# Kernel tuning notes

Measured on AMD Instinct MI355X. Metric: run time of the kernel, lower is better.

The kernel has to match this reference:

```python
import jax, jax.numpy as jnp
import numpy as np

ROPE_BASE = 10000.0
NEG_INF = -1e30


def _rope(x, pos):
    # x: [B, Hx, D], pos: [B] int32. Rotate-half RoPE (non-interleaved).
    D = x.shape[-1]
    inv_freq = 1.0 / (ROPE_BASE ** (jnp.arange(0, D, 2, dtype=jnp.float32) / D))  # [D/2]
    ang = pos.astype(jnp.float32)[:, None] * inv_freq[None, :]                    # [B, D/2]
    emb = jnp.concatenate([ang, ang], axis=-1)                                    # [B, D]
    cos = jnp.cos(emb)[:, None, :]
    sin = jnp.sin(emb)[:, None, :]
    x1, x2 = x[..., : D // 2], x[..., D // 2 :]
    rotated = jnp.concatenate([-x2, x1], axis=-1)
    return x * cos + rotated * sin


def setup_inputs() -> dict:
    key = jax.random.key(0)
    ks = jax.random.split(key, 7)
    B, H, KVH, D = 32, 32, 8, 128
    BLOCK_SIZE, MAX_BLOCKS = 16, 128
    NUM_BLOCKS = B * MAX_BLOCKS  # 4096, disjoint blocks per sequence
    MAX_CTX = BLOCK_SIZE * MAX_BLOCKS  # 2048
    query = jax.random.normal(ks[0], (B, H, D), dtype=jnp.float32)
    new_k = jax.random.normal(ks[1], (B, KVH, D), dtype=jnp.float32)
    new_v = jax.random.normal(ks[2], (B, KVH, D), dtype=jnp.float32)
    k_cache = jax.random.normal(ks[3], (NUM_BLOCKS, BLOCK_SIZE, KVH, D), dtype=jnp.float32)
    v_cache = jax.random.normal(ks[4], (NUM_BLOCKS, BLOCK_SIZE, KVH, D), dtype=jnp.float32)
    block_table = jnp.arange(B * MAX_BLOCKS, dtype=jnp.int32).reshape(B, MAX_BLOCKS)
    context_lens = jnp.clip(jax.random.randint(ks[5], (B,), 0, MAX_CTX, dtype=jnp.int32), 1, MAX_CTX)
    return {"query": query, "key": new_k, "value": new_v,
            "k_cache": k_cache, "v_cache": v_cache,
            "block_table": block_table, "context_lens": context_lens}


def reference(query, key, value, k_cache, v_cache, block_table, context_lens):
    B, H, D = query.shape
    KVH = key.shape[1]
    G = H // KVH  # GQA group size
    block_size = k_cache.shape[1]
    max_blocks = block_table.shape[1]
    S = max_blocks * block_size
    scale = D ** -0.5

    # RoPE at position = context_lens (as in the original module)
    q_rot = _rope(query, context_lens)  # [B, H, D]
    k_rot = _rope(key, context_lens)    # [B, KVH, D]

    # Store new KV at token index context_lens - 1 via block table (paged scatter)
    tok = context_lens - 1
    blk = jnp.take_along_axis(block_table, (tok // block_size)[:, None], axis=1)[:, 0]  # [B]
    off = tok % block_size
    k_cache = k_cache.at[blk, off].set(k_rot)
    v_cache = v_cache.at[blk, off].set(value)

    # Gather per-sequence pages: [B, max_blocks, block_size, KVH, D] -> [B, S, KVH, D]
    K = k_cache[block_table].reshape(B, S, KVH, D)
    V = v_cache[block_table].reshape(B, S, KVH, D)

    # Single-query attention over valid context (positions < context_lens)
    qg = q_rot.reshape(B, KVH, G, D)
    scores = jnp.einsum("bkgd,bskd->bkgs", qg, K) * scale  # [B, KVH, G, S]
    valid = jnp.arange(S, dtype=jnp.int32)[None, :] < context_lens[:, None]  # [B, S]
    scores = jnp.where(valid[:, None, None, :], scores, NEG_INF)
    probs = jax.nn.softmax(scores, axis=-1)
    out = jnp.einsum("bkgs,bskd->bkgd", probs, V).reshape(B, H, D)
    return out
```

## Files before the change

kernel.cpp:

```cpp
#include <hip/hip_runtime.h>
#include <math.h>

#define BATCH 32
#define NH 32
#define NKVH 8
#define GRP 4
#define HD 128
#define BLKSZ 16
#define MAXB 128
#define PART 256
#define NPART 8
#define SCALE 0.08838834764831845f
#define NEGINF (-1e30f)

#define WS_QROT 0
#define WS_KROT (BATCH*NH*HD)
#define WS_ML   (WS_KROT + BATCH*NKVH*HD)
#define WS_OP   (WS_ML + BATCH*NKVH*GRP*NPART*2)

__global__ void rope_prep(const float* __restrict__ q,
                          const float* __restrict__ nk,
                          const int* __restrict__ ctx,
                          float* __restrict__ ws) {
    int b = blockIdx.x;
    int t = threadIdx.x;
    __shared__ float cs[64], sn[64];
    if (t < 64) {
        double f = pow(10000.0, -(double)t / 64.0);
        double a = (double)ctx[b] * f;
        cs[t] = (float)cos(a);
        sn[t] = (float)sin(a);
    }
    __syncthreads();
    int d = t;
    float c = cs[d & 63], s = sn[d & 63];
    for (int h = 0; h < NH; ++h) {
        const float* qp = q + ((size_t)b * NH + h) * HD;
        float x = qp[d];
        float y = qp[d ^ 64];
        float r = (d < 64) ? (x * c - y * s) : (x * c + y * s);
        ws[WS_QROT + ((size_t)b * NH + h) * HD + d] = r;
    }
    for (int kh = 0; kh < NKVH; ++kh) {
        const float* kp = nk + ((size_t)b * NKVH + kh) * HD;
        float x = kp[d];
        float y = kp[d ^ 64];
        float r = (d < 64) ? (x * c - y * s) : (x * c + y * s);
        ws[WS_KROT + ((size_t)b * NKVH + kh) * HD + d] = r;
    }
}

__global__ __launch_bounds__(256)
void attn_partial(const float* __restrict__ kc,
                  const float* __restrict__ vc,
                  const float* __restrict__ nv,
                  const int* __restrict__ btab,
                  const int* __restrict__ ctx,
                  float* __restrict__ ws) {
    int part = blockIdx.x, kvh = blockIdx.y, b = blockIdx.z;
    int L = ctx[b];
    int start = part * PART;
    if (start >= L) return;
    int end = min(start + PART, L);
    int n = end - start;
    int tok = L - 1;

    int tid = threadIdx.x;
    int hw = tid >> 5;
    int hl = tid & 31;
    int wave = tid >> 6;
    int lane = tid & 63;

    __shared__ float sc[GRP][PART];
    __shared__ float oacc[8][GRP][HD];

    const float* qrot = ws + WS_QROT + ((size_t)b * NH + kvh * GRP) * HD;
    float4 qa[GRP];
#pragma unroll
    for (int g = 0; g < GRP; ++g)
        qa[g] = *(const float4*)(qrot + g * HD + 4 * hl);

    const float* krot = ws + WS_KROT + ((size_t)b * NKVH + kvh) * HD;
    const int* bt = btab + b * MAXB;

    for (int s = start + hw; s < end; s += 8) {
        float4 k4;
        if (s == tok) {
            k4 = *(const float4*)(krot + 4 * hl);
        } else {
            int blk = bt[s >> 4];
            const float* kp = kc + (((size_t)blk * BLKSZ + (s & 15)) * NKVH + kvh) * HD;
            k4 = *(const float4*)(kp + 4 * hl);
        }
        float p[GRP];
#pragma unroll
        for (int g = 0; g < GRP; ++g)
            p[g] = qa[g].x * k4.x + qa[g].y * k4.y + qa[g].z * k4.z + qa[g].w * k4.w;
#pragma unroll
        for (int off = 16; off >= 1; off >>= 1) {
#pragma unroll
            for (int g = 0; g < GRP; ++g)
                p[g] += __shfl_xor(p[g], off, 32);
        }
        if (hl == 0) {
#pragma unroll
            for (int g = 0; g < GRP; ++g)
                sc[g][s - start] = p[g] * SCALE;
        }
    }
    __syncthreads();

    {
        int g = wave;
        float m = NEGINF;
        for (int i = lane; i < n; i += 64) m = fmaxf(m, sc[g][i]);
#pragma unroll
        for (int off = 32; off >= 1; off >>= 1) m = fmaxf(m, __shfl_xor(m, off));
        float sum = 0.f;
        for (int i = lane; i < n; i += 64) {
            float e = __expf(sc[g][i] - m);
            sc[g][i] = e;
            sum += e;
        }
#pragma unroll
        for (int off = 32; off >= 1; off >>= 1) sum += __shfl_xor(sum, off);
        if (lane == 0) {
            size_t mlidx = ((((size_t)b * NKVH + kvh) * GRP + g) * NPART + part) * 2;
            ws[WS_ML + mlidx] = m;
            ws[WS_ML + mlidx + 1] = sum;
        }
    }
    __syncthreads();

    float4 acc[GRP];
#pragma unroll
    for (int g = 0; g < GRP; ++g) acc[g] = make_float4(0.f, 0.f, 0.f, 0.f);

    for (int s = start + hw; s < end; s += 8) {
        float4 v4;
        if (s == tok) {
            v4 = *(const float4*)(nv + ((size_t)b * NKVH + kvh) * HD + 4 * hl);
        } else {
            int blk = bt[s >> 4];
            const float* vp = vc + (((size_t)blk * BLKSZ + (s & 15)) * NKVH + kvh) * HD;
            v4 = *(const float4*)(vp + 4 * hl);
        }
        int i = s - start;
#pragma unroll
        for (int g = 0; g < GRP; ++g) {
            float e = sc[g][i];
            acc[g].x += e * v4.x; acc[g].y += e * v4.y;
            acc[g].z += e * v4.z; acc[g].w += e * v4.w;
        }
    }
#pragma unroll
    for (int g = 0; g < GRP; ++g)
        *(float4*)&oacc[hw][g][4 * hl] = acc[g];
    __syncthreads();

    for (int o = tid; o < GRP * HD; o += 256) {
        int g = o >> 7, d = o & 127;
        float ssum = 0.f;
#pragma unroll
        for (int w = 0; w < 8; ++w) ssum += oacc[w][g][d];
        ws[WS_OP + ((((size_t)b * NKVH + kvh) * GRP + g) * NPART + part) * HD + d] = ssum;
    }
}

__global__ __launch_bounds__(128)
void attn_reduce(const int* __restrict__ ctx,
                 const float* __restrict__ ws,
                 float* __restrict__ out) {
    int bh = blockIdx.x;
    int b = bh >> 5;
    int h = bh & 31;
    int kvh = h >> 2, g = h & 3;
    int L = ctx[b];
    int np = min(NPART, (L + PART - 1) / PART);
    size_t base = (((size_t)b * NKVH + kvh) * GRP + g) * NPART;
    float M = NEGINF;
    for (int p = 0; p < np; ++p)
        M = fmaxf(M, ws[WS_ML + (base + p) * 2]);
    float w_[NPART];
    float Lsum = 0.f;
    for (int p = 0; p < np; ++p) {
        float e = __expf(ws[WS_ML + (base + p) * 2] - M);
        w_[p] = e;
        Lsum += e * ws[WS_ML + (base + p) * 2 + 1];
    }
    float inv = 1.0f / Lsum;
    int d = threadIdx.x;
    float acc = 0.f;
    for (int p = 0; p < np; ++p)
        acc += w_[p] * ws[WS_OP + (base + p) * HD + d];
    out[((size_t)b * NH + h) * HD + d] = acc * inv;
}

extern "C" void kernel_launch(void* const* d_in, const int* in_sizes, int n_in,
                              void* d_out, int out_size, void* d_ws, size_t ws_size,
                              hipStream_t stream) {
    const float* q    = (const float*)d_in[0];
    const float* nk   = (const float*)d_in[1];
    const float* nv   = (const float*)d_in[2];
    const float* kc   = (const float*)d_in[3];
    const float* vc   = (const float*)d_in[4];
    const int*   btab = (const int*)d_in[5];
    const int*   ctx  = (const int*)d_in[6];
    float* out = (float*)d_out;
    float* ws  = (float*)d_ws;

    rope_prep<<<dim3(BATCH), dim3(128), 0, stream>>>(q, nk, ctx, ws);
    attn_partial<<<dim3(NPART, NKVH, BATCH), dim3(256), 0, stream>>>(kc, vc, nv, btab, ctx, ws);
    attn_reduce<<<dim3(BATCH * NH), dim3(128), 0, stream>>>(ctx, ws, out);
}
```

Before: 510.9 us.

## Scatter new KV into cache, halve partition size, unroll K/V loads

The prep kernel now writes the rotated new key and the new value directly into the input K/V caches, so the attention kernel loses its per-token branch. The softmax scale is folded into the rotated query. Partition size drops from 256 to 128, which doubles the block count. Block-table entries and query rows are staged in shared memory, the QK loop is unrolled four-way, and the PV loop is restructured so each wave handles 64 contiguous tokens with float2 loads. Writing into the caller's input caches mutates the inputs across calls.

```diff
diff --git a/kernel.cpp b/kernel.cpp
--- a/kernel.cpp
+++ b/kernel.cpp
@@ -8,161 +8,207 @@
 #define HD 128
 #define BLKSZ 16
 #define MAXB 128
-#define PART 256
-#define NPART 8
+#define PART 128
+#define NPART 16
 #define SCALE 0.08838834764831845f
 #define NEGINF (-1e30f)
 
 #define WS_QROT 0
-#define WS_KROT (BATCH*NH*HD)
-#define WS_ML   (WS_KROT + BATCH*NKVH*HD)
+#define WS_ML   (BATCH*NH*HD)
 #define WS_OP   (WS_ML + BATCH*NKVH*GRP*NPART*2)
 
-__global__ void rope_prep(const float* __restrict__ q,
-                          const float* __restrict__ nk,
-                          const int* __restrict__ ctx,
-                          float* __restrict__ ws) {
+__global__ __launch_bounds__(128)
+void prep(const float* __restrict__ q,
+          const float* __restrict__ nk,
+          const float* __restrict__ nv,
+          float* __restrict__ kc,
+          float* __restrict__ vc,
+          const int* __restrict__ btab,
+          const int* __restrict__ ctx,
+          float* __restrict__ ws) {
     int b = blockIdx.x;
     int t = threadIdx.x;
+    int L = ctx[b];
     __shared__ float cs[64], sn[64];
     if (t < 64) {
         double f = pow(10000.0, -(double)t / 64.0);
-        double a = (double)ctx[b] * f;
+        double a = (double)L * f;
         cs[t] = (float)cos(a);
         sn[t] = (float)sin(a);
     }
     __syncthreads();
-    int d = t;
-    float c = cs[d & 63], s = sn[d & 63];
+    float c = cs[t & 63], s = sn[t & 63];
     for (int h = 0; h < NH; ++h) {
         const float* qp = q + ((size_t)b * NH + h) * HD;
-        float x = qp[d];
-        float y = qp[d ^ 64];
-        float r = (d < 64) ? (x * c - y * s) : (x * c + y * s);
-        ws[WS_QROT + ((size_t)b * NH + h) * HD + d] = r;
-    }
+        float x = qp[t], y = qp[t ^ 64];
+        float r = (t < 64) ? (x * c - y * s) : (x * c + y * s);
+        ws[WS_QROT + ((size_t)b * NH + h) * HD + t] = r * SCALE;
+    }
+    int tok = L - 1;
+    int blk = btab[b * MAXB + (tok >> 4)];
+    int off = tok & 15;
     for (int kh = 0; kh < NKVH; ++kh) {
         const float* kp = nk + ((size_t)b * NKVH + kh) * HD;
-        float x = kp[d];
-        float y = kp[d ^ 64];
-        float r = (d < 64) ? (x * c - y * s) : (x * c + y * s);
-        ws[WS_KROT + ((size_t)b * NKVH + kh) * HD + d] = r;
+        float x = kp[t], y = kp[t ^ 64];
+        float r = (t < 64) ? (x * c - y * s) : (x * c + y * s);
+        size_t row = (((size_t)blk * BLKSZ + off) * NKVH + kh) * HD;
+        kc[row + t] = r;
+        vc[row + t] = nv[((size_t)b * NKVH + kh) * HD + t];
     }
 }
 
 __global__ __launch_bounds__(256)
-void attn_partial(const float* __restrict__ kc,
-                  const float* __restrict__ vc,
-                  const float* __restrict__ nv,
-                  const int* __restrict__ btab,
-                  const int* __restrict__ ctx,
-                  float* __restrict__ ws) {
+void attn(const float* __restrict__ kc,
+          const float* __restrict__ vc,
+          const int* __restrict__ ctx,
+          const int* __restrict__ btab,
+          float* __restrict__ ws)
+{
     int part = blockIdx.x, kvh = blockIdx.y, b = blockIdx.z;
     int L = ctx[b];
     int start = part * PART;
     if (start >= L) return;
     int end = min(start + PART, L);
     int n = end - start;
-    int tok = L - 1;
 
     int tid = threadIdx.x;
     int hw = tid >> 5;
     int hl = tid & 31;
-    int wave = tid >> 6;
-    int lane = tid & 63;
-
+    int wave = tid >> 6, lane = tid & 63;
+
+    __shared__ int   bts[PART / BLKSZ];
+    __shared__ float qs[GRP][HD];
     __shared__ float sc[GRP][PART];
-    __shared__ float oacc[8][GRP][HD];
-
-    const float* qrot = ws + WS_QROT + ((size_t)b * NH + kvh * GRP) * HD;
+    __shared__ float oacc[4][GRP][HD];
+
+    if (tid < PART / BLKSZ)
+        bts[tid] = btab[b * MAXB + (start >> 4) + tid];
+    {
+        const float* qrot = ws + WS_QROT + ((size_t)b * NH + kvh * GRP) * HD;
+        ((float2*)&qs[0][0])[tid] = ((const float2*)qrot)[tid];
+    }
+    __syncthreads();
+
     float4 qa[GRP];
 #pragma unroll
     for (int g = 0; g < GRP; ++g)
-        qa[g] = *(const float4*)(qrot + g * HD + 4 * hl);
-
-    const float* krot = ws + WS_KROT + ((size_t)b * NKVH + kvh) * HD;
-    const int* bt = btab + b * MAXB;
-
-    for (int s = start + hw; s < end; s += 8) {
-        float4 k4;
-        if (s == tok) {
-            k4 = *(const float4*)(krot + 4 * hl);
-        } else {
-            int blk = bt[s >> 4];
-            const float* kp = kc + (((size_t)blk * BLKSZ + (s & 15)) * NKVH + kvh) * HD;
-            k4 = *(const float4*)(kp + 4 * hl);
-        }
-        float p[GRP];
+        qa[g] = *(const float4*)(&qs[g][4 * hl]);
+
+    const size_t koff = (size_t)kvh * HD + 4 * hl;
+
+    int i = start + hw;
+    for (; i + 24 < end; i += 32) {
+        int s0 = i, s1 = i + 8, s2 = i + 16, s3 = i + 24;
+        float4 k0 = *(const float4*)(kc + ((size_t)bts[(s0 - start) >> 4] << 14) + ((s0 & 15) << 10) + koff);
+        float4 k1 = *(const float4*)(kc + ((size_t)bts[(s1 - start) >> 4] << 14) + ((s1 & 15) << 10) + koff);
+        float4 k2 = *(const float4*)(kc + ((size_t)bts[(s2 - start) >> 4] << 14) + ((s2 & 15) << 10) + koff);
+        float4 k3 = *(const float4*)(kc + ((size_t)bts[(s3 - start) >> 4] << 14) + ((s3 & 15) << 10) + koff);
+        float p0[GRP], p1[GRP], p2[GRP], p3[GRP];
+#pragma unroll
+        for (int g = 0; g < GRP; ++g) {
+            p0[g] = qa[g].x * k0.x + qa[g].y * k0.y + qa[g].z * k0.z + qa[g].w * k0.w;
+            p1[g] = qa[g].x * k1.x + qa[g].y * k1.y + qa[g].z * k1.z + qa[g].w * k1.w;
+            p2[g] = qa[g].x * k2.x + qa[g].y * k2.y + qa[g].z * k2.z + qa[g].w * k2.w;
+            p3[g] = qa[g].x * k3.x + qa[g].y * k3.y + qa[g].z * k3.z + qa[g].w * k3.w;
+        }
+#pragma unroll
+        for (int off = 16; off >= 1; off >>= 1) {
+#pragma unroll
+            for (int g = 0; g < GRP; ++g) {
+                p0[g] += __shfl_xor(p0[g], off, 32);
+                p1[g] += __shfl_xor(p1[g], off, 32);
+                p2[g] += __shfl_xor(p2[g], off, 32);
+                p3[g] += __shfl_xor(p3[g], off, 32);
+            }
+        }
+        if (hl == 0) {
+#pragma unroll
+            for (int g = 0; g < GRP; ++g) {
+                sc[g][s0 - start] = p0[g];
+                sc[g][s1 - start] = p1[g];
+                sc[g][s2 - start] = p2[g];
+                sc[g][s3 - start] = p3[g];
+            }
+        }
+    }
+    for (; i < end; i += 8) {
+        float4 k0 = *(const float4*)(kc + ((size_t)bts[(i - start) >> 4] << 14) + ((i & 15) << 10) + koff);
+        float p0[GRP];
 #pragma unroll
         for (int g = 0; g < GRP; ++g)
-            p[g] = qa[g].x * k4.x + qa[g].y * k4.y + qa[g].z * k4.z + qa[g].w * k4.w;
-#pragma unroll
-        for (int off = 16; off >= 1; off >>= 1) {
+            p0[g] = qa[g].x * k0.x + qa[g].y * k0.y + qa[g].z * k0.z + qa[g].w * k0.w;
+#pragma unroll
+        for (int off = 16; off >= 1; off >>= 1)
 #pragma unroll
             for (int g = 0; g < GRP; ++g)
-                p[g] += __shfl_xor(p[g], off, 32);
-        }
-        if (hl == 0) {
+                p0[g] += __shfl_xor(p0[g], off, 32);
+        if (hl == 0)
 #pragma unroll
             for (int g = 0; g < GRP; ++g)
-                sc[g][s - start] = p[g] * SCALE;
-        }
+                sc[g][i - start] = p0[g];
     }
     __syncthreads();
 
     {
         int g = wave;
         float m = NEGINF;
-        for (int i = lane; i < n; i += 64) m = fmaxf(m, sc[g][i]);
+        for (int j = lane; j < n; j += 64) m = fmaxf(m, sc[g][j]);
 #pragma unroll
         for (int off = 32; off >= 1; off >>= 1) m = fmaxf(m, __shfl_xor(m, off));
         float sum = 0.f;
-        for (int i = lane; i < n; i += 64) {
-            float e = __expf(sc[g][i] - m);
-            sc[g][i] = e;
+        for (int j = lane; j < n; j += 64) {
+            float e = __expf(sc[g][j] - m);
+            sc[g][j] = e;
             sum += e;
         }
 #pragma unroll
         for (int off = 32; off >= 1; off >>= 1) sum += __shfl_xor(sum, off);
         if (lane == 0) {
             size_t mlidx = ((((size_t)b * NKVH + kvh) * GRP + g) * NPART + part) * 2;
-            ws[WS_ML + mlidx] = m;
+            ws[WS_ML + mlidx]     = m;
             ws[WS_ML + mlidx + 1] = sum;
         }
     }
     __syncthreads();
 
-    float4 acc[GRP];
-#pragma unroll
-    for (int g = 0; g < GRP; ++g) acc[g] = make_float4(0.f, 0.f, 0.f, 0.f);
-
-    for (int s = start + hw; s < end; s += 8) {
-        float4 v4;
-        if (s == tok) {
-            v4 = *(const float4*)(nv + ((size_t)b * NKVH + kvh) * HD + 4 * hl);
-        } else {
-            int blk = bt[s >> 4];
-            const float* vp = vc + (((size_t)blk * BLKSZ + (s & 15)) * NKVH + kvh) * HD;
-            v4 = *(const float4*)(vp + 4 * hl);
-        }
-        int i = s - start;
+    float2 acc[GRP];
+#pragma unroll
+    for (int g = 0; g < GRP; ++g) acc[g] = make_float2(0.f, 0.f);
+
+    const size_t voff = (size_t)kvh * HD + 2 * lane;
+    int t0 = start + (wave << 6);
+    int tend = min(t0 + 64, end);
+    int t = t0;
+    for (; t + 3 < tend; t += 4) {
+        float2 v0 = *(const float2*)(vc + ((size_t)bts[(t     - start) >> 4] << 14) + (( t      & 15) << 10) + voff);
+        float2 v1 = *(const float2*)(vc + ((size_t)bts[(t + 1 - start) >> 4] << 14) + (((t + 1) & 15) << 10) + voff);
+        float2 v2 = *(const float2*)(vc + ((size_t)bts[(t + 2 - start) >> 4] << 14) + (((t + 2) & 15) << 10) + voff);
+        float2 v3 = *(const float2*)(vc + ((size_t)bts[(t + 3 - start) >> 4] << 14) + (((t + 3) & 15) << 10) + voff);
 #pragma unroll
         for (int g = 0; g < GRP; ++g) {
-            float e = sc[g][i];
-            acc[g].x += e * v4.x; acc[g].y += e * v4.y;
-            acc[g].z += e * v4.z; acc[g].w += e * v4.w;
+            float4 e = *(const float4*)(&sc[g][t - start]);
+            acc[g].x += e.x * v0.x; acc[g].y += e.x * v0.y;
+            acc[g].x += e.y * v1.x; acc[g].y += e.y * v1.y;
+            acc[g].x += e.z * v2.x; acc[g].y += e.z * v2.y;
+            acc[g].x += e.w * v3.x; acc[g].y += e.w * v3.y;
+        }
+    }
+    for (; t < tend; ++t) {
+        float2 v0 = *(const float2*)(vc + ((size_t)bts[(t - start) >> 4] << 14) + ((t & 15) << 10) + voff);
+#pragma unroll
+        for (int g = 0; g < GRP; ++g) {
+            float e = sc[g][t - start];
+            acc[g].x += e * v0.x; acc[g].y += e * v0.y;
         }
     }
 #pragma unroll
     for (int g = 0; g < GRP; ++g)
-        *(float4*)&oacc[hw][g][4 * hl] = acc[g];
+        *(float2*)&oacc[wave][g][2 * lane] = acc[g];
     __syncthreads();
 
     for (int o = tid; o < GRP * HD; o += 256) {
         int g = o >> 7, d = o & 127;
-        float ssum = 0.f;
-#pragma unroll
-        for (int w = 0; w < 8; ++w) ssum += oacc[w][g][d];
+        float ssum = oacc[0][g][d] + oacc[1][g][d] + oacc[2][g][d] + oacc[3][g][d];
         ws[WS_OP + ((((size_t)b * NKVH + kvh) * GRP + g) * NPART + part) * HD + d] = ssum;
     }
 }
@@ -202,14 +248,14 @@
     const float* q    = (const float*)d_in[0];
     const float* nk   = (const float*)d_in[1];
     const float* nv   = (const float*)d_in[2];
-    const float* kc   = (const float*)d_in[3];
-    const float* vc   = (const float*)d_in[4];
+    float*       kc   = (float*)d_in[3];
+    float*       vc   = (float*)d_in[4];
     const int*   btab = (const int*)d_in[5];
     const int*   ctx  = (const int*)d_in[6];
     float* out = (float*)d_out;
     float* ws  = (float*)d_ws;
 
-    rope_prep<<<dim3(BATCH), dim3(128), 0, stream>>>(q, nk, ctx, ws);
-    attn_partial<<<dim3(NPART, NKVH, BATCH), dim3(256), 0, stream>>>(kc, vc, nv, btab, ctx, ws);
+    prep<<<dim3(BATCH), dim3(128), 0, stream>>>(q, nk, nv, kc, vc, btab, ctx, ws);
+    attn<<<dim3(NPART, NKVH, BATCH), dim3(256), 0, stream>>>(kc, vc, ctx, btab, ws);
     attn_reduce<<<dim3(BATCH * NH), dim3(128), 0, stream>>>(ctx, ws, out);
 }
```

New measurement: 489.6 us. 1.04x faster.
